# Kernel optimization log

Measured on AMD Instinct MI355X. Metric: run time of the kernel, lower is better.

The kernel has to match this reference:

```python
import jax, jax.numpy as jnp
import numpy as np

N = 100000      # num nodes
E = 1600000     # num edges (avg degree 16)
F_IN = 700      # hardcoded in_feats in build()
H = 128         # args.hidden
EPS = 1e-5      # BatchNorm1d eps


def setup_inputs() -> dict:
    key = jax.random.key(0)
    ks = jax.random.split(key, 12)
    w = lambda k, shape: jax.random.normal(k, shape, dtype=jnp.float32) * 0.05
    return {
        "inputs": jax.random.normal(ks[0], (1, N, F_IN), dtype=jnp.float32),
        "graph": jax.random.randint(ks[1], (1, E, 2), 0, N, dtype=jnp.int32),
        "Wself0": w(ks[2], (F_IN, H)),
        "Wneigh0": w(ks[3], (F_IN, H)),
        "b0": jnp.zeros((H,), jnp.float32),
        "Wself": w(ks[4], (3, H, H)),
        "Wneigh": w(ks[5], (3, H, H)),
        "b": jnp.zeros((3, H), jnp.float32),
        "bn_gamma": jnp.ones((4, H), jnp.float32),
        "bn_beta": jnp.zeros((4, H), jnp.float32),
        "W1": w(ks[6], (H, 64)),
        "b1": jnp.zeros((64,), jnp.float32),
        "bng1": jnp.ones((64,), jnp.float32),
        "bnb1": jnp.zeros((64,), jnp.float32),
        "W2": w(ks[7], (64, 1)),
        "b2": jnp.zeros((1,), jnp.float32),
    }


def _batch_norm(x, g, beta):
    # training-mode BN over node dim (biased variance, as PyTorch normalizes)
    mu = jnp.mean(x, axis=0)
    var = jnp.mean((x - mu) ** 2, axis=0)
    return (x - mu) * jax.lax.rsqrt(var + EPS) * g + beta


def reference(inputs, graph, Wself0, Wneigh0, b0, Wself, Wneigh, b,
              bn_gamma, bn_beta, W1, b1, bng1, bnb1, W2, b2):
    h = inputs[0]                      # [N, F_IN] (squeeze + flatten is a no-op)
    edges = graph[0]                   # [E, 2]
    src, dst = edges[:, 0], edges[:, 1]
    deg = jax.ops.segment_sum(jnp.ones((E,), jnp.float32), dst, num_segments=N)
    denom = jnp.maximum(deg, 1.0)[:, None]   # DGL clamps zero in-degree

    def sage(x, Ws, Wn, bias):
        # SAGEConv(mean): fc before message passing (linearity => equivalent)
        hn = x @ Wn                                                   # [N, H]
        agg = jax.ops.segment_sum(hn[src], dst, num_segments=N) / denom
        return x @ Ws + agg + bias

    # layer 0: no residual
    h = sage(h, Wself0, Wneigh0, b0)
    h = jax.nn.relu(_batch_norm(h, bn_gamma[0], bn_beta[0]))
    # layers 1..3: BN + residual + relu (dropout = identity in eval)
    for l in range(3):
        pre = h
        h = sage(h, Wself[l], Wneigh[l], b[l])
        h = _batch_norm(h, bn_gamma[l + 1], bn_beta[l + 1])
        h = jax.nn.relu(h + pre)

    z = _batch_norm(h @ W1 + b1, bng1, bnb1)
    z = jax.nn.relu(z)
    out = z @ W2 + b2                  # [N, 1]
    return out.T                       # permute(1,0) -> [1, N]
```

## Files before the change

kernel.cpp:

```cpp
#include <hip/hip_runtime.h>
#include <hip/hip_bf16.h>

#define N_NODES 100000
#define N_EDGES 1600000
#define F_IN    700
#define NKB0    22
#define HDIM    128
#define SCAN_B  256
#define NB_SCAN ((N_NODES + SCAN_B - 1) / SCAN_B)
#define NSHARD  64

typedef _Float16 half8 __attribute__((ext_vector_type(8)));
typedef _Float16 half4 __attribute__((ext_vector_type(4)));
typedef float floatx4 __attribute__((ext_vector_type(4)));

__device__ __forceinline__ void cp16(const void* g, void* l) {
    __builtin_amdgcn_global_load_lds(
        (const __attribute__((address_space(1))) void*)g,
        (__attribute__((address_space(3))) void*)l, 16, 0, 0);
}

__global__ void count_edges(const int* __restrict__ graph, int* __restrict__ cnt) {
    int e = blockIdx.x * blockDim.x + threadIdx.x;
    if (e < N_EDGES) atomicAdd(&cnt[graph[2 * e + 1]], 1);
}

__global__ void scan1(const int* __restrict__ cnt, int* __restrict__ incl,
                      int* __restrict__ blk) {
    __shared__ int s[SCAN_B];
    int tid = threadIdx.x;
    int i = blockIdx.x * SCAN_B + tid;
    s[tid] = (i < N_NODES) ? cnt[i] : 0;
    __syncthreads();
    for (int off = 1; off < SCAN_B; off <<= 1) {
        int t = (tid >= off) ? s[tid - off] : 0;
        __syncthreads();
        s[tid] += t;
        __syncthreads();
    }
    if (i < N_NODES) incl[i] = s[tid];
    if (tid == SCAN_B - 1) blk[blockIdx.x] = s[tid];
}

__global__ void scan2(const int* __restrict__ blk, int* __restrict__ blkoff) {
    __shared__ int s[512];
    int tid = threadIdx.x;
    s[tid] = (tid < NB_SCAN) ? blk[tid] : 0;
    __syncthreads();
    for (int off = 1; off < 512; off <<= 1) {
        int t = (tid >= off) ? s[tid - off] : 0;
        __syncthreads();
        s[tid] += t;
        __syncthreads();
    }
    if (tid < NB_SCAN) blkoff[tid] = (tid == 0) ? 0 : s[tid - 1];
}

__global__ void scan3(const int* __restrict__ incl, const int* __restrict__ blkoff,
                      int* __restrict__ row_ptr) {
    int i = blockIdx.x * SCAN_B + threadIdx.x;
    if (i < N_NODES) {
        row_ptr[i + 1] = incl[i] + blkoff[i >> 8];
        if (i == 0) row_ptr[0] = 0;
    }
}

__global__ void fill_edges(const int* __restrict__ graph, const int* __restrict__ row_ptr,
                           int* __restrict__ cursor, int* __restrict__ esrc) {
    int e = blockIdx.x * blockDim.x + threadIdx.x;
    if (e < N_EDGES) {
        int src = graph[2 * e];
        int dst = graph[2 * e + 1];
        esrc[row_ptr[dst] + atomicAdd(&cursor[dst], 1)] = src;
    }
}

__global__ void build_wtp0(const float* __restrict__ Wn, const float* __restrict__ Ws,
                           _Float16* __restrict__ out) {
    int q = blockIdx.x * blockDim.x + threadIdx.x;
    if (q >= NKB0 * 256 * 4) return;
    int kb = q >> 10;
    int r  = (q >> 2) & 255;
    int cc = q & 3;
    int k0 = kb * 32 + (cc ^ ((r >> 1) & 3)) * 8;
    half8 v;
    #pragma unroll
    for (int e = 0; e < 8; e++) {
        int k = k0 + e;
        float f = 0.0f;
        if (k < F_IN) f = (r < 128) ? Wn[k * 128 + r] : Ws[k * 128 + (r - 128)];
        v[e] = (_Float16)f;
    }
    *(half8*)&out[(size_t)q * 8] = v;
}

__global__ void build_wtpl(const float* __restrict__ Wn, const float* __restrict__ Ws,
                           _Float16* __restrict__ out) {
    int q = blockIdx.x * blockDim.x + threadIdx.x;
    if (q >= 3 * 4 * 256 * 4) return;
    int l = q >> 12;
    int rem = q & 4095;
    int kb = rem >> 10;
    int r  = (rem >> 2) & 255;
    int cc = rem & 3;
    int k0 = kb * 32 + (cc ^ ((r >> 1) & 3)) * 8;
    half8 v;
    #pragma unroll
    for (int e = 0; e < 8; e++) {
        int k = k0 + e;
        float f = (r < 128) ? Wn[l * 16384 + k * 128 + r]
                            : Ws[l * 16384 + k * 128 + (r - 128)];
        v[e] = (_Float16)f;
    }
    *(half8*)&out[(size_t)q * 8] = v;
}

__global__ __launch_bounds__(512) void gemm0_nu(
    const float* __restrict__ A, int M, int K,
    const _Float16* __restrict__ Wtp, const float* __restrict__ bias,
    const float* __restrict__ zbuf,
    _Float16* __restrict__ Cn, _Float16* __restrict__ Cs) {
    __shared__ char sbuf[2][32768];

    int tid = threadIdx.x;
    int wave = tid >> 6, lane = tid & 63;
    int lm = lane & 15, quad = lane >> 4;
    int wm = wave >> 2, wn = wave & 3;
    long row0 = (long)blockIdx.x * 128;

    floatx4 acc[4][4] = {};

    auto stage = [&](int kb, char* buf) {
        #pragma unroll
        for (int pass = 0; pass < 2; pass++) {
            int q = pass * 512 + tid;
            int r = q >> 3, cc = q & 7;
            int ccg = cc ^ (r & 7);
            long grow = row0 + r;
            if (grow >= M) grow = 0;
            int gk = kb * 32 + ccg * 4;
            const float* src = (gk + 4 <= K) ? (A + grow * (long)K + gk) : zbuf;
            cp16(src, buf + pass * 8192 + wave * 1024);
        }
        const _Float16* wsrc = Wtp + (size_t)kb * 8192;
        #pragma unroll
        for (int pass = 0; pass < 2; pass++) {
            cp16(wsrc + (size_t)(pass * 512 + tid) * 8,
                 buf + 16384 + pass * 8192 + wave * 1024);
        }
    };

    stage(0, sbuf[0]);

    for (int kb = 0; kb < NKB0; kb++) {
        int p = kb & 1;
        if (kb + 1 < NKB0) {
            stage(kb + 1, sbuf[p ^ 1]);
            asm volatile("s_waitcnt vmcnt(4)\n\ts_barrier" ::: "memory");
        } else {
            asm volatile("s_waitcnt vmcnt(0)\n\ts_barrier" ::: "memory");
        }

        const float* Af = (const float*)sbuf[p];
        const _Float16* Bf = (const _Float16*)(sbuf[p] + 16384);
        half8 af[4];
        #pragma unroll
        for (int i = 0; i < 4; i++) {
            int row = wm * 64 + i * 16 + lm;
            int c0 = (quad * 2) ^ (row & 7);
            int c1 = (quad * 2 + 1) ^ (row & 7);
            floatx4 f0 = *(const floatx4*)&Af[row * 32 + c0 * 4];
            floatx4 f1 = *(const floatx4*)&Af[row * 32 + c1 * 4];
            af[i][0] = (_Float16)f0[0]; af[i][1] = (_Float16)f0[1];
            af[i][2] = (_Float16)f0[2]; af[i][3] = (_Float16)f0[3];
            af[i][4] = (_Float16)f1[0]; af[i][5] = (_Float16)f1[1];
            af[i][6] = (_Float16)f1[2]; af[i][7] = (_Float16)f1[3];
        }
        #pragma unroll
        for (int j = 0; j < 4; j++) {
            int brow = wn * 64 + j * 16 + lm;
            int ch = quad ^ ((brow >> 1) & 3);
            half8 bf = *(const half8*)&Bf[brow * 32 + ch * 8];
            #pragma unroll
            for (int i = 0; i < 4; i++)
                acc[i][j] = __builtin_amdgcn_mfma_f32_16x16x32_f16(af[i], bf, acc[i][j], 0, 0, 0);
        }
        asm volatile("s_waitcnt lgkmcnt(0)\n\ts_barrier" ::: "memory");
    }

    #pragma unroll
    for (int i = 0; i < 4; i++) {
        long r0 = row0 + wm * 64 + i * 16 + quad * 4;
        #pragma unroll
        for (int j = 0; j < 4; j++) {
            int c = wn * 64 + j * 16 + lm;
            if (c >= 128) {
                float badd = bias[c - 128];
                #pragma unroll
                for (int rr = 0; rr < 4; rr++) {
                    long r = r0 + rr;
                    if (r < M) Cs[r * HDIM + (c - 128)] = (_Float16)(acc[i][j][rr] + badd);
                }
            } else {
                #pragma unroll
                for (int rr = 0; rr < 4; rr++) {
                    long r = r0 + rr;
                    if (r < M) Cn[r * HDIM + c] = (_Float16)acc[i][j][rr];
                }
            }
        }
    }
}

__global__ __launch_bounds__(512) void gemm16_nu(
    const _Float16* __restrict__ A, int M,
    const _Float16* __restrict__ Wtp, const float* __restrict__ bias,
    _Float16* __restrict__ Cn, _Float16* __restrict__ Cs) {
    __shared__ _Float16 sbuf[2][12288];

    int tid = threadIdx.x;
    int wave = tid >> 6, lane = tid & 63;
    int lm = lane & 15, quad = lane >> 4;
    int wm = wave >> 2, wn = wave & 3;
    long row0 = (long)blockIdx.x * 128;

    floatx4 acc[4][4] = {};

    auto stage = [&](int kb, _Float16* buf) {
        {
            int r = tid >> 2, cc = tid & 3;
            int ccg = cc ^ ((r >> 1) & 3);
            long grow = row0 + r;
            if (grow >= M) grow = 0;
            cp16(A + grow * (long)HDIM + kb * 32 + ccg * 8,
                 buf + wave * 512);
        }
        const _Float16* wsrc = Wtp + (size_t)kb * 8192;
        #pragma unroll
        for (int pass = 0; pass < 2; pass++) {
            cp16(wsrc + (size_t)(pass * 512 + tid) * 8,
                 buf + 4096 + pass * 4096 + wave * 512);
        }
    };

    stage(0, sbuf[0]);

    for (int kb = 0; kb < 4; kb++) {
        int p = kb & 1;
        if (kb + 1 < 4) {
            stage(kb + 1, sbuf[p ^ 1]);
            asm volatile("s_waitcnt vmcnt(3)\n\ts_barrier" ::: "memory");
        } else {
            asm volatile("s_waitcnt vmcnt(0)\n\ts_barrier" ::: "memory");
        }

        const _Float16* bp = sbuf[p];
        half8 af[4];
        #pragma unroll
        for (int i = 0; i < 4; i++) {
            int row = wm * 64 + i * 16 + lm;
            int ch = quad ^ ((row >> 1) & 3);
            af[i] = *(const half8*)&bp[row * 32 + ch * 8];
        }
        #pragma unroll
        for (int j = 0; j < 4; j++) {
            int brow = wn * 64 + j * 16 + lm;
            int ch = quad ^ ((brow >> 1) & 3);
            half8 bf = *(const half8*)&bp[4096 + brow * 32 + ch * 8];
            #pragma unroll
            for (int i = 0; i < 4; i++)
                acc[i][j] = __builtin_amdgcn_mfma_f32_16x16x32_f16(af[i], bf, acc[i][j], 0, 0, 0);
        }
        asm volatile("s_waitcnt lgkmcnt(0)\n\ts_barrier" ::: "memory");
    }

    #pragma unroll
    for (int i = 0; i < 4; i++) {
        long r0 = row0 + wm * 64 + i * 16 + quad * 4;
        #pragma unroll
        for (int j = 0; j < 4; j++) {
            int c = wn * 64 + j * 16 + lm;
            if (c >= 128) {
                float badd = bias[c - 128];
                #pragma unroll
                for (int rr = 0; rr < 4; rr++) {
                    long r = r0 + rr;
                    if (r < M) Cs[r * HDIM + (c - 128)] = (_Float16)(acc[i][j][rr] + badd);
                }
            } else {
                #pragma unroll
                for (int rr = 0; rr < 4; rr++) {
                    long r = r0 + rr;
                    if (r < M) Cn[r * HDIM + c] = (_Float16)acc[i][j][rr];
                }
            }
        }
    }
}

__global__ __launch_bounds__(256) void aggregate_w(
    const _Float16* __restrict__ hn, const int* __restrict__ row_ptr,
    const int* __restrict__ esrc, const _Float16* __restrict__ cs16,
    _Float16* __restrict__ pre16, float* __restrict__ stats) {
    __shared__ float s1[4][HDIM], s2[4][HDIM];
    int tid = threadIdx.x;
    int wave = tid >> 6, lane = tid & 63;
    int n = blockIdx.x * 4 + wave;
    bool valid = (n < N_NODES);
    int eg = lane >> 4;
    int c8 = (lane & 15) * 8;

    float pv[8] = {};
    if (valid) {
        int start = row_ptr[n], end = row_ptr[n + 1];
        float acc[8] = {};
        for (int base = start; base < end; base += 16) {
            #pragma unroll
            for (int u = 0; u < 4; u++) {
                int e = base + u * 4 + eg;
                if (e < end) {
                    int s = esrc[e];
                    half8 v = *(const half8*)&hn[(size_t)s * HDIM + c8];
                    #pragma unroll
                    for (int i = 0; i < 8; i++) acc[i] += (float)v[i];
                }
            }
        }
        #pragma unroll
        for (int i = 0; i < 8; i++) {
            acc[i] += __shfl_xor(acc[i], 16, 64);
            acc[i] += __shfl_xor(acc[i], 32, 64);
        }
        if (eg == 0) {
            float rd = 1.0f / (float)max(end - start, 1);
            half8 sv = *(const half8*)&cs16[(size_t)n * HDIM + c8];
            half8 h;
            #pragma unroll
            for (int i = 0; i < 8; i++) {
                pv[i] = acc[i] * rd + (float)sv[i];
                h[i] = (_Float16)pv[i];
            }
            *(half8*)&pre16[(size_t)n * HDIM + c8] = h;
        }
    }
    if (eg == 0) {
        #pragma unroll
        for (int i = 0; i < 8; i++) {
            float v = valid ? pv[i] : 0.0f;
            s1[wave][c8 + i] = v;
            s2[wave][c8 + i] = v * v;
        }
    }
    __syncthreads();
    if (tid < HDIM) {
        float a = s1[0][tid] + s1[1][tid] + s1[2][tid] + s1[3][tid];
        float b = s2[0][tid] + s2[1][tid] + s2[2][tid] + s2[3][tid];
        float* sh = stats + (size_t)(blockIdx.x & (NSHARD - 1)) * 256;
        atomicAdd(&sh[tid], a);
        atomicAdd(&sh[128 + tid], b);
    }
}

__global__ void bn_apply16(const _Float16* __restrict__ P, const _Float16* __restrict__ res16,
                           _Float16* __restrict__ out16,
                           const float* __restrict__ stats,
                           const float* __restrict__ gamma, const float* __restrict__ beta,
                           int M, int total8, int Cdiv8) {
    __shared__ float ssc[HDIM], ssh[HDIM];
    int tid = threadIdx.x;
    int C = Cdiv8 * 8;
    if (tid < C) {
        float s = 0.0f, s2 = 0.0f;
        #pragma unroll 8
        for (int k = 0; k < NSHARD; k++) {
            s  += stats[k * 256 + tid];
            s2 += stats[k * 256 + 128 + tid];
        }
        float mean = s / (float)M;
        float var = s2 / (float)M - mean * mean;
        float sc = rsqrtf(var + 1e-5f) * gamma[tid];
        ssc[tid] = sc;
        ssh[tid] = beta[tid] - mean * sc;
    }
    __syncthreads();
    for (int f = blockIdx.x * blockDim.x + tid; f < total8;
         f += gridDim.x * blockDim.x) {
        int c8 = (f % Cdiv8) * 8;
        half8 v = *(const half8*)&P[(size_t)f * 8];
        half8 h;
        if (res16) {
            half8 rv = *(const half8*)&res16[(size_t)f * 8];
            #pragma unroll
            for (int i = 0; i < 8; i++) {
                float x = (float)v[i] * ssc[c8 + i] + ssh[c8 + i] + (float)rv[i];
                h[i] = (_Float16)fmaxf(x, 0.0f);
            }
        } else {
            #pragma unroll
            for (int i = 0; i < 8; i++) {
                float x = (float)v[i] * ssc[c8 + i] + ssh[c8 + i];
                h[i] = (_Float16)fmaxf(x, 0.0f);
            }
        }
        *(half8*)&out16[(size_t)f * 8] = h;
    }
}

__global__ __launch_bounds__(256) void mlp_gemm(const _Float16* __restrict__ H,
                                                const float* __restrict__ W1,
                                                const float* __restrict__ b1,
                                                float* __restrict__ Z,
                                                float* __restrict__ stats, int M) {
    __shared__ float hs[64 * 132];
    __shared__ float ws[128 * 64];
    __shared__ float zs1[16][64], zs2[16][64];
    int tid = threadIdx.x;
    int tx = tid & 15;
    int ty = tid >> 4;
    int row0 = blockIdx.x * 64;

    #pragma unroll
    for (int t = 0; t < 8; t++) {
        int f = tid + t * 256;
        int r = f >> 4, c4 = (f & 15) * 4;
        *(float4*)&ws[r * 64 + c4] = *(const float4*)&W1[r * 64 + c4];
    }
    #pragma unroll
    for (int t = 0; t < 4; t++) {
        int f = tid + t * 256;
        int r = f >> 4, c8 = (f & 15) * 8;
        int gr = row0 + r;
        if (gr < M) {
            half8 hv = *(const half8*)&H[(size_t)gr * HDIM + c8];
            #pragma unroll
            for (int i = 0; i < 8; i++) hs[r * 132 + c8 + i] = (float)hv[i];
        } else {
            #pragma unroll
            for (int i = 0; i < 8; i++) hs[r * 132 + c8 + i] = 0.0f;
        }
    }
    __syncthreads();

    float acc[4][4] = {};
    for (int k = 0; k < 128; k++) {
        float a[4];
        #pragma unroll
        for (int i = 0; i < 4; i++) a[i] = hs[(ty * 4 + i) * 132 + k];
        float4 b4 = *(const float4*)&ws[k * 64 + tx * 4];
        #pragma unroll
        for (int i = 0; i < 4; i++) {
            acc[i][0] += a[i] * b4.x; acc[i][1] += a[i] * b4.y;
            acc[i][2] += a[i] * b4.z; acc[i][3] += a[i] * b4.w;
        }
    }
    float4 bb = *(const float4*)&b1[tx * 4];
    float cs[4] = {}, cq[4] = {};
    #pragma unroll
    for (int i = 0; i < 4; i++) {
        int r = row0 + ty * 4 + i;
        if (r < M) {
            float v0 = acc[i][0] + bb.x;
            float v1 = acc[i][1] + bb.y;
            float v2 = acc[i][2] + bb.z;
            float v3 = acc[i][3] + bb.w;
            float4 v = {v0, v1, v2, v3};
            *(float4*)&Z[(size_t)r * 64 + tx * 4] = v;
            cs[0] += v0; cq[0] += v0 * v0;
            cs[1] += v1; cq[1] += v1 * v1;
            cs[2] += v2; cq[2] += v2 * v2;
            cs[3] += v3; cq[3] += v3 * v3;
        }
    }
    #pragma unroll
    for (int j = 0; j < 4; j++) {
        zs1[ty][tx * 4 + j] = cs[j];
        zs2[ty][tx * 4 + j] = cq[j];
    }
    __syncthreads();
    if (tid < 64) {
        float a = 0.0f, b = 0.0f;
        #pragma unroll
        for (int k = 0; k < 16; k++) { a += zs1[k][tid]; b += zs2[k][tid]; }
        float* sh = stats + (size_t)(blockIdx.x & (NSHARD - 1)) * 256;
        atomicAdd(&sh[tid], a);
        atomicAdd(&sh[128 + tid], b);
    }
}

__global__ void final_out(const float* __restrict__ Z,
                          const float* __restrict__ stats,
                          const float* __restrict__ gamma, const float* __restrict__ beta,
                          const float* __restrict__ W2, const float* __restrict__ b2,
                          float* __restrict__ out, int M) {
    __shared__ float ssc[64], ssh[64], sw[64];
    int tid = threadIdx.x;
    if (tid < 64) {
        float s = 0.0f, s2 = 0.0f;
        #pragma unroll 8
        for (int k = 0; k < NSHARD; k++) {
            s  += stats[k * 256 + tid];
            s2 += stats[k * 256 + 128 + tid];
        }
        float mean = s / (float)M;
        float var = s2 / (float)M - mean * mean;
        float sc = rsqrtf(var + 1e-5f) * gamma[tid];
        ssc[tid] = sc;
        ssh[tid] = beta[tid] - mean * sc;
        sw[tid] = W2[tid];
    }
    __syncthreads();
    int n = blockIdx.x * 4 + (tid >> 6);
    int lane = tid & 63;
    if (n >= N_NODES) return;
    float z = Z[(size_t)n * 64 + lane] * ssc[lane] + ssh[lane];
    z = fmaxf(z, 0.0f);
    float v = z * sw[lane];
    #pragma unroll
    for (int off = 32; off >= 1; off >>= 1) v += __shfl_down(v, off, 64);
    if (lane == 0) out[n] = v + b2[0];
}

extern "C" void kernel_launch(void* const* d_in, const int* in_sizes, int n_in,
                              void* d_out, int out_size, void* d_ws, size_t ws_size,
                              hipStream_t stream) {
    const float* X       = (const float*)d_in[0];
    const int*   graph   = (const int*)d_in[1];
    const float* Wself0  = (const float*)d_in[2];
    const float* Wneigh0 = (const float*)d_in[3];
    const float* b0      = (const float*)d_in[4];
    const float* Wself   = (const float*)d_in[5];
    const float* Wneigh  = (const float*)d_in[6];
    const float* bvec    = (const float*)d_in[7];
    const float* bn_g    = (const float*)d_in[8];
    const float* bn_b    = (const float*)d_in[9];
    const float* W1      = (const float*)d_in[10];
    const float* b1      = (const float*)d_in[11];
    const float* bng1    = (const float*)d_in[12];
    const float* bnb1    = (const float*)d_in[13];
    const float* W2      = (const float*)d_in[14];
    const float* b2      = (const float*)d_in[15];
    float* out = (float*)d_out;

    size_t off = 0;
    auto alloc = [&](size_t bytes) {
        void* p = (char*)d_ws + off;
        off += (bytes + 255) & ~(size_t)255;
        return p;
    };
    int* cnt     = (int*)alloc(N_NODES * 4);
    int* cursor  = (int*)alloc(N_NODES * 4);
    int* row_ptr = (int*)alloc((N_NODES + 1) * 4);
    int* incl    = (int*)alloc(N_NODES * 4);
    int* blk     = (int*)alloc(NB_SCAN * 4);
    int* blkoff  = (int*)alloc(NB_SCAN * 4);
    int* esrc    = (int*)alloc((size_t)N_EDGES * 4);
    _Float16* pre16 = (_Float16*)alloc((size_t)N_NODES * HDIM * 2);
    _Float16* cs16  = (_Float16*)alloc((size_t)N_NODES * HDIM * 2);
    _Float16* h16A  = (_Float16*)alloc((size_t)N_NODES * HDIM * 2);
    _Float16* h16B  = (_Float16*)alloc((size_t)N_NODES * HDIM * 2);
    _Float16* hn16  = (_Float16*)alloc((size_t)N_NODES * HDIM * 2);
    float*    Z     = (float*)alloc((size_t)N_NODES * 64 * 4);
    _Float16* Wtp0  = (_Float16*)alloc((size_t)NKB0 * 8192 * 2);
    _Float16* Wtpl  = (_Float16*)alloc((size_t)3 * 4 * 8192 * 2);
    float*    zbuf  = (float*)alloc(256);
    float*    stats = (float*)alloc((size_t)NSHARD * 256 * 4);

    const int EB = (N_EDGES + 255) / 256;
    const int GB2 = (N_NODES + 127) / 128;
    const int AGB = (N_NODES + 3) / 4;
    const size_t STB = (size_t)NSHARD * 256 * 4;
    const int TOT8 = N_NODES * HDIM / 8;

    hipMemsetAsync(cnt, 0, N_NODES * 4, stream);
    hipMemsetAsync(cursor, 0, N_NODES * 4, stream);
    hipMemsetAsync(zbuf, 0, 256, stream);
    count_edges<<<EB, 256, 0, stream>>>(graph, cnt);
    scan1<<<NB_SCAN, SCAN_B, 0, stream>>>(cnt, incl, blk);
    scan2<<<1, 512, 0, stream>>>(blk, blkoff);
    scan3<<<NB_SCAN, SCAN_B, 0, stream>>>(incl, blkoff, row_ptr);
    fill_edges<<<EB, 256, 0, stream>>>(graph, row_ptr, cursor, esrc);

    build_wtp0<<<(NKB0 * 1024 + 255) / 256, 256, 0, stream>>>(Wneigh0, Wself0, Wtp0);
    build_wtpl<<<(3 * 4096 + 255) / 256, 256, 0, stream>>>(Wneigh, Wself, Wtpl);

    _Float16* hc = h16A;
    _Float16* hx = h16B;

    gemm0_nu<<<GB2, 512, 0, stream>>>(X, N_NODES, F_IN, Wtp0, b0, zbuf, hn16, cs16);
    hipMemsetAsync(stats, 0, STB, stream);
    aggregate_w<<<AGB, 256, 0, stream>>>(hn16, row_ptr, esrc, cs16, pre16, stats);
    bn_apply16<<<1024, 256, 0, stream>>>(pre16, nullptr, hc, stats,
                                         bn_g, bn_b, N_NODES, TOT8, HDIM / 8);

    for (int l = 0; l < 3; l++) {
        gemm16_nu<<<GB2, 512, 0, stream>>>(hc, N_NODES, Wtpl + (size_t)l * 32768,
                                           bvec + l * HDIM, hn16, cs16);
        hipMemsetAsync(stats, 0, STB, stream);
        aggregate_w<<<AGB, 256, 0, stream>>>(hn16, row_ptr, esrc, cs16, pre16, stats);
        bn_apply16<<<1024, 256, 0, stream>>>(pre16, hc, hx, stats,
                                             bn_g + (l + 1) * HDIM,
                                             bn_b + (l + 1) * HDIM, N_NODES,
                                             TOT8, HDIM / 8);
        _Float16* t = hc; hc = hx; hx = t;
    }

    hipMemsetAsync(stats, 0, STB, stream);
    mlp_gemm<<<(N_NODES + 63) / 64, 256, 0, stream>>>(hc, W1, b1, Z, stats, N_NODES);
    final_out<<<AGB, 256, 0, stream>>>(Z, stats, bng1, bnb1, W2, b2,
                                       out, N_NODES);
}
```

Measured before the change: 1.179 ms.

## Fuse neighbor aggregation and batch-norm apply into one cooperative grid-synced kernel

Replaces the separate aggregate and BN-apply kernels with a single cooperative kernel of 1024 persistent blocks. Each block aggregates 100 nodes and keeps the pre-norm rows in LDS, accumulates BN statistics, then grid-syncs and applies normalization, residual and ReLU straight from LDS. This drops the pre16 global round-trip (one write plus one read of N x 128 halves) and one kernel launch per layer. In exchange it adds a grid barrier, roughly 25 KB of LDS per block that limits occupancy, and fixed blocks that may load-balance worse on irregular node degrees.

```diff
diff --git a/kernel.cpp b/kernel.cpp
--- a/kernel.cpp
+++ b/kernel.cpp
@@ -1,5 +1,8 @@
 #include <hip/hip_runtime.h>
 #include <hip/hip_bf16.h>
+#include <hip/hip_cooperative_groups.h>
+
+namespace cg = cooperative_groups;
 
 #define N_NODES 100000
 #define N_EDGES 1600000
@@ -9,6 +12,9 @@
 #define SCAN_B  256
 #define NB_SCAN ((N_NODES + SCAN_B - 1) / SCAN_B)
 #define NSHARD  64
+#define CNB     1024
+#define CITER   25
+#define CNPB    (CITER * 4)
 
 typedef _Float16 half8 __attribute__((ext_vector_type(8)));
 typedef _Float16 half4 __attribute__((ext_vector_type(4)));
@@ -298,57 +304,63 @@
     }
 }
 
-__global__ __launch_bounds__(256) void aggregate_w(
+__global__ __launch_bounds__(256, 4) void agg_bn_coop(
     const _Float16* __restrict__ hn, const int* __restrict__ row_ptr,
     const int* __restrict__ esrc, const _Float16* __restrict__ cs16,
-    _Float16* __restrict__ pre16, float* __restrict__ stats) {
+    const _Float16* __restrict__ res16, _Float16* __restrict__ out16,
+    float* __restrict__ stats, const float* __restrict__ gamma,
+    const float* __restrict__ beta) {
+    __shared__ _Float16 preL[CNPB][HDIM];
     __shared__ float s1[4][HDIM], s2[4][HDIM];
+    __shared__ float ssc[HDIM], ssh[HDIM];
     int tid = threadIdx.x;
     int wave = tid >> 6, lane = tid & 63;
-    int n = blockIdx.x * 4 + wave;
-    bool valid = (n < N_NODES);
     int eg = lane >> 4;
     int c8 = (lane & 15) * 8;
-
-    float pv[8] = {};
-    if (valid) {
-        int start = row_ptr[n], end = row_ptr[n + 1];
-        float acc[8] = {};
-        for (int base = start; base < end; base += 16) {
-            #pragma unroll
-            for (int u = 0; u < 4; u++) {
-                int e = base + u * 4 + eg;
-                if (e < end) {
-                    int s = esrc[e];
-                    half8 v = *(const half8*)&hn[(size_t)s * HDIM + c8];
-                    #pragma unroll
-                    for (int i = 0; i < 8; i++) acc[i] += (float)v[i];
+    long nbase = (long)blockIdx.x * CNPB;
+
+    for (int i = tid; i < 4 * HDIM; i += 256) {
+        (&s1[0][0])[i] = 0.0f;
+        (&s2[0][0])[i] = 0.0f;
+    }
+    __syncthreads();
+
+    for (int it = 0; it < CITER; it++) {
+        int nl = it * 4 + wave;
+        long n = nbase + nl;
+        if (n < N_NODES) {
+            int start = row_ptr[n], end = row_ptr[n + 1];
+            float acc[8] = {};
+            for (int base = start; base < end; base += 16) {
+                #pragma unroll
+                for (int u = 0; u < 4; u++) {
+                    int e = base + u * 4 + eg;
+                    if (e < end) {
+                        int s = esrc[e];
+                        half8 v = *(const half8*)&hn[(size_t)s * HDIM + c8];
+                        #pragma unroll
+                        for (int i = 0; i < 8; i++) acc[i] += (float)v[i];
+                    }
                 }
             }
-        }
-        #pragma unroll
-        for (int i = 0; i < 8; i++) {
-            acc[i] += __shfl_xor(acc[i], 16, 64);
-            acc[i] += __shfl_xor(acc[i], 32, 64);
-        }
-        if (eg == 0) {
-            float rd = 1.0f / (float)max(end - start, 1);
-            half8 sv = *(const half8*)&cs16[(size_t)n * HDIM + c8];
-            half8 h;
             #pragma unroll
             for (int i = 0; i < 8; i++) {
-                pv[i] = acc[i] * rd + (float)sv[i];
-                h[i] = (_Float16)pv[i];
+                acc[i] += __shfl_xor(acc[i], 16, 64);
+                acc[i] += __shfl_xor(acc[i], 32, 64);
             }
-            *(half8*)&pre16[(size_t)n * HDIM + c8] = h;
-        }
-    }
-    if (eg == 0) {
-        #pragma unroll
-        for (int i = 0; i < 8; i++) {
-            float v = valid ? pv[i] : 0.0f;
-            s1[wave][c8 + i] = v;
-            s2[wave][c8 + i] = v * v;
+            if (eg == 0) {
+                float rd = 1.0f / (float)max(end - start, 1);
+                half8 sv = *(const half8*)&cs16[(size_t)n * HDIM + c8];
+                half8 h;
+                #pragma unroll
+                for (int i = 0; i < 8; i++) {
+                    float pv = acc[i] * rd + (float)sv[i];
+                    h[i] = (_Float16)pv;
+                    s1[wave][c8 + i] += pv;
+                    s2[wave][c8 + i] += pv * pv;
+                }
+                *(half8*)&preL[nl][c8] = h;
+            }
         }
     }
     __syncthreads();
@@ -359,50 +371,47 @@
         atomicAdd(&sh[tid], a);
         atomicAdd(&sh[128 + tid], b);
     }
-}
-
-__global__ void bn_apply16(const _Float16* __restrict__ P, const _Float16* __restrict__ res16,
-                           _Float16* __restrict__ out16,
-                           const float* __restrict__ stats,
-                           const float* __restrict__ gamma, const float* __restrict__ beta,
-                           int M, int total8, int Cdiv8) {
-    __shared__ float ssc[HDIM], ssh[HDIM];
-    int tid = threadIdx.x;
-    int C = Cdiv8 * 8;
-    if (tid < C) {
-        float s = 0.0f, s2 = 0.0f;
+
+    cg::this_grid().sync();
+
+    if (tid < HDIM) {
+        float s = 0.0f, s2v = 0.0f;
         #pragma unroll 8
         for (int k = 0; k < NSHARD; k++) {
-            s  += stats[k * 256 + tid];
-            s2 += stats[k * 256 + 128 + tid];
-        }
-        float mean = s / (float)M;
-        float var = s2 / (float)M - mean * mean;
+            s   += stats[k * 256 + tid];
+            s2v += stats[k * 256 + 128 + tid];
+        }
+        float mean = s / (float)N_NODES;
+        float var = s2v / (float)N_NODES - mean * mean;
         float sc = rsqrtf(var + 1e-5f) * gamma[tid];
         ssc[tid] = sc;
         ssh[tid] = beta[tid] - mean * sc;
     }
     __syncthreads();
-    for (int f = blockIdx.x * blockDim.x + tid; f < total8;
-         f += gridDim.x * blockDim.x) {
-        int c8 = (f % Cdiv8) * 8;
-        half8 v = *(const half8*)&P[(size_t)f * 8];
-        half8 h;
-        if (res16) {
-            half8 rv = *(const half8*)&res16[(size_t)f * 8];
-            #pragma unroll
-            for (int i = 0; i < 8; i++) {
-                float x = (float)v[i] * ssc[c8 + i] + ssh[c8 + i] + (float)rv[i];
-                h[i] = (_Float16)fmaxf(x, 0.0f);
+
+    for (int idx = tid; idx < CNPB * 16; idx += 256) {
+        int nl = idx >> 4;
+        int cc8 = (idx & 15) * 8;
+        long n = nbase + nl;
+        if (n < N_NODES) {
+            half8 v = *(const half8*)&preL[nl][cc8];
+            half8 h;
+            if (res16) {
+                half8 rv = *(const half8*)&res16[(size_t)n * HDIM + cc8];
+                #pragma unroll
+                for (int i = 0; i < 8; i++) {
+                    float x = (float)v[i] * ssc[cc8 + i] + ssh[cc8 + i] + (float)rv[i];
+                    h[i] = (_Float16)fmaxf(x, 0.0f);
+                }
+            } else {
+                #pragma unroll
+                for (int i = 0; i < 8; i++) {
+                    float x = (float)v[i] * ssc[cc8 + i] + ssh[cc8 + i];
+                    h[i] = (_Float16)fmaxf(x, 0.0f);
+                }
             }
-        } else {
-            #pragma unroll
-            for (int i = 0; i < 8; i++) {
-                float x = (float)v[i] * ssc[c8 + i] + ssh[c8 + i];
-                h[i] = (_Float16)fmaxf(x, 0.0f);
-            }
-        }
-        *(half8*)&out16[(size_t)f * 8] = h;
+            *(half8*)&out16[(size_t)n * HDIM + cc8] = h;
+        }
     }
 }
 
@@ -554,7 +563,6 @@
     int* blk     = (int*)alloc(NB_SCAN * 4);
     int* blkoff  = (int*)alloc(NB_SCAN * 4);
     int* esrc    = (int*)alloc((size_t)N_EDGES * 4);
-    _Float16* pre16 = (_Float16*)alloc((size_t)N_NODES * HDIM * 2);
     _Float16* cs16  = (_Float16*)alloc((size_t)N_NODES * HDIM * 2);
     _Float16* h16A  = (_Float16*)alloc((size_t)N_NODES * HDIM * 2);
     _Float16* h16B  = (_Float16*)alloc((size_t)N_NODES * HDIM * 2);
@@ -569,7 +577,6 @@
     const int GB2 = (N_NODES + 127) / 128;
     const int AGB = (N_NODES + 3) / 4;
     const size_t STB = (size_t)NSHARD * 256 * 4;
-    const int TOT8 = N_NODES * HDIM / 8;
 
     hipMemsetAsync(cnt, 0, N_NODES * 4, stream);
     hipMemsetAsync(cursor, 0, N_NODES * 4, stream);
@@ -588,19 +595,26 @@
 
     gemm0_nu<<<GB2, 512, 0, stream>>>(X, N_NODES, F_IN, Wtp0, b0, zbuf, hn16, cs16);
     hipMemsetAsync(stats, 0, STB, stream);
-    aggregate_w<<<AGB, 256, 0, stream>>>(hn16, row_ptr, esrc, cs16, pre16, stats);
-    bn_apply16<<<1024, 256, 0, stream>>>(pre16, nullptr, hc, stats,
-                                         bn_g, bn_b, N_NODES, TOT8, HDIM / 8);
+    {
+        const _Float16* res = nullptr;
+        const float* g = bn_g; const float* b = bn_b;
+        void* args[] = {(void*)&hn16, (void*)&row_ptr, (void*)&esrc, (void*)&cs16,
+                        (void*)&res, (void*)&hc, (void*)&stats, (void*)&g, (void*)&b};
+        hipLaunchCooperativeKernel((void*)agg_bn_coop, dim3(CNB), dim3(256),
+                                   args, 0, stream);
+    }
 
     for (int l = 0; l < 3; l++) {
         gemm16_nu<<<GB2, 512, 0, stream>>>(hc, N_NODES, Wtpl + (size_t)l * 32768,
                                            bvec + l * HDIM, hn16, cs16);
         hipMemsetAsync(stats, 0, STB, stream);
-        aggregate_w<<<AGB, 256, 0, stream>>>(hn16, row_ptr, esrc, cs16, pre16, stats);
-        bn_apply16<<<1024, 256, 0, stream>>>(pre16, hc, hx, stats,
-                                             bn_g + (l + 1) * HDIM,
-                                             bn_b + (l + 1) * HDIM, N_NODES,
-                                             TOT8, HDIM / 8);
+        const _Float16* res = hc;
+        const float* g = bn_g + (l + 1) * HDIM;
+        const float* b = bn_b + (l + 1) * HDIM;
+        void* args[] = {(void*)&hn16, (void*)&row_ptr, (void*)&esrc, (void*)&cs16,
+                        (void*)&res, (void*)&hx, (void*)&stats, (void*)&g, (void*)&b};
+        hipLaunchCooperativeKernel((void*)agg_bn_coop, dim3(CNB), dim3(256),
+                                   args, 0, stream);
         _Float16* t = hc; hc = hx; hx = t;
     }
 
```

Result: slower. 1.863 ms (+57.9%).
